# Performance work log

Measured on AMD Instinct MI355X. Metric: run time of the kernel, lower is better.

Reference implementation:

```python
import jax, jax.numpy as jnp
import numpy as np

# Multi-scale deformable attention (MSDeformableAttention from RTDETRTransformerv2)
SPATIAL = ((80, 80), (40, 40), (20, 20))  # (h, w) per level, strides 8/16/32 on 640x640
N_HEADS, N_LEVELS, N_POINTS = 8, 3, 4
D_MODEL = 256
HEAD_DIM = D_MODEL // N_HEADS


def setup_inputs() -> dict:
    key = jax.random.key(0)
    ks = jax.random.split(key, 10)
    B, Q = 16, 300
    Lv = sum(h * w for h, w in SPATIAL)  # 8400
    s = 0.02
    return {
        "query": jax.random.normal(ks[0], (B, Q, D_MODEL), jnp.float32),
        "reference_points": jax.random.uniform(ks[1], (B, Q, 4), jnp.float32),
        "value": jax.random.normal(ks[2], (B, Lv, D_MODEL), jnp.float32),
        "Wv": jax.random.normal(ks[3], (D_MODEL, D_MODEL), jnp.float32) * s,
        "bv": jnp.zeros((D_MODEL,), jnp.float32),
        "Woff": jax.random.normal(ks[4], (D_MODEL, N_HEADS * N_LEVELS * N_POINTS * 2), jnp.float32) * s,
        "boff": jax.random.normal(ks[5], (N_HEADS * N_LEVELS * N_POINTS * 2,), jnp.float32) * 0.1,
        "Wattn": jax.random.normal(ks[6], (D_MODEL, N_HEADS * N_LEVELS * N_POINTS), jnp.float32) * s,
        "battn": jnp.zeros((N_HEADS * N_LEVELS * N_POINTS,), jnp.float32),
        "Wout": jax.random.normal(ks[7], (D_MODEL, D_MODEL), jnp.float32) * s,
        "bout": jnp.zeros((D_MODEL,), jnp.float32),
    }


def _grid_sample_level(v_lvl, gx, gy, h, w):
    """Bilinear grid_sample, align_corners=False, zeros padding.

    v_lvl : (B, nH, h*w, hd) flattened per-level value map
    gx,gy : (B, nH, P) sample coords in [-1, 1]
    returns (B, nH, P, hd)
    """
    px = ((gx + 1.0) * w - 1.0) * 0.5  # pixel x
    py = ((gy + 1.0) * h - 1.0) * 0.5  # pixel y
    x0 = jnp.floor(px)
    y0 = jnp.floor(py)
    fx = px - x0
    fy = py - y0
    x0i = x0.astype(jnp.int32)
    y0i = y0.astype(jnp.int32)

    def corner(xi, yi, wgt):
        valid = (xi >= 0) & (xi < w) & (yi >= 0) & (yi < h)
        idx = jnp.clip(yi, 0, h - 1) * w + jnp.clip(xi, 0, w - 1)
        g = jnp.take_along_axis(v_lvl, idx[..., None], axis=2)  # (B,nH,P,hd)
        return g * (wgt * valid.astype(wgt.dtype))[..., None]

    return (corner(x0i, y0i, (1 - fx) * (1 - fy))
            + corner(x0i + 1, y0i, fx * (1 - fy))
            + corner(x0i, y0i + 1, (1 - fx) * fy)
            + corner(x0i + 1, y0i + 1, fx * fy))


def reference(query, reference_points, value, Wv, bv, Woff, boff, Wattn, battn, Wout, bout):
    B, Q, _ = query.shape
    # value projection -> per-head values
    v = (value @ Wv + bv).reshape(B, -1, N_HEADS, HEAD_DIM)
    # sampling offsets and attention weights from queries
    off = (query @ Woff + boff).reshape(B, Q, N_HEADS, N_LEVELS, N_POINTS, 2)
    aw = jax.nn.softmax(
        (query @ Wattn + battn).reshape(B, Q, N_HEADS, N_LEVELS * N_POINTS), axis=-1
    ).reshape(B, Q, N_HEADS, N_LEVELS, N_POINTS)
    # reference points (cx, cy) broadcast over heads/levels/points
    ref = reference_points[:, :, None, None, None, :2]
    pts = jnp.clip(ref + off, 0.0, 1.0)      # (B,Q,nH,nL,nP,2) in [0,1]
    g = pts * 2.0 - 1.0                      # grid_sample coords in [-1,1]

    out = jnp.zeros((B, Q, N_HEADS, HEAD_DIM), query.dtype)
    start = 0
    for lvl, (h, w) in enumerate(SPATIAL):
        v_lvl = v[:, start:start + h * w].transpose(0, 2, 1, 3)  # (B,nH,hw,hd)
        gl = g[:, :, :, lvl]                                     # (B,Q,nH,nP,2)
        gx = gl[..., 0].transpose(0, 2, 1, 3).reshape(B, N_HEADS, Q * N_POINTS)
        gy = gl[..., 1].transpose(0, 2, 1, 3).reshape(B, N_HEADS, Q * N_POINTS)
        sampled = _grid_sample_level(v_lvl, gx, gy, h, w)        # (B,nH,Q*nP,hd)
        sampled = sampled.reshape(B, N_HEADS, Q, N_POINTS, HEAD_DIM)
        wl = aw[:, :, :, lvl].transpose(0, 2, 1, 3)              # (B,nH,Q,nP)
        out = out + jnp.einsum('bhqpd,bhqp->bqhd', sampled, wl)
        start += h * w

    return out.reshape(B, Q, D_MODEL) @ Wout + bout
```

## Files before the change

kernel.cpp:

```cpp
#include <hip/hip_runtime.h>
#include <hip/hip_bf16.h>
#include <cstddef>

#define NB 16
#define NQ 300
#define DM 256
#define LV_ 8400

typedef __attribute__((ext_vector_type(8))) short short8;
typedef __attribute__((ext_vector_type(4))) float f32x4;

static __device__ __forceinline__ unsigned short bf16_rne(float f) {
  unsigned int u = __builtin_bit_cast(unsigned int, f);
  u += 0x7FFFu + ((u >> 16) & 1u);
  return (unsigned short)(u >> 16);
}

static __device__ __forceinline__ unsigned int pack_bf2(float a, float b) {
  __hip_bfloat162 p = __float22bfloat162_rn(make_float2(a, b));
  unsigned int u;
  __builtin_memcpy(&u, &p, 4);
  return u;
}

__global__ __launch_bounds__(256) void prep_kernel(
    const float* __restrict__ Wv, const float* __restrict__ Wout,
    unsigned short* __restrict__ Wth, unsigned short* __restrict__ WoutT) {
  const float* src = blockIdx.z ? Wout : Wv;
  unsigned short* dst = blockIdx.z ? WoutT : Wth;
  __shared__ float tle[32][33];
  const int k0 = blockIdx.x * 32, n0 = blockIdx.y * 32;
  const int xx = threadIdx.x & 31, y4 = (threadIdx.x >> 5) * 4;
  #pragma unroll
  for (int i = 0; i < 4; ++i)
    tle[y4 + i][xx] = src[(size_t)(k0 + y4 + i) * DM + n0 + xx];
  __syncthreads();
  #pragma unroll
  for (int i = 0; i < 4; ++i)
    dst[(size_t)(n0 + y4 + i) * DM + k0 + xx] = bf16_rne(tle[xx][y4 + i]);
}

__global__ __launch_bounds__(256) void vproj_mfma(
    const float* __restrict__ A, const unsigned short* __restrict__ Wth,
    const float* __restrict__ bias, unsigned short* __restrict__ V) {
  __shared__ short Ah[4][128][8];
  __shared__ short Bh[4][128][8];
  const int tid = threadIdx.x;
  const int lane = tid & 63;
  const int wave = tid >> 6;
  const int l16 = lane & 15, q4 = lane >> 4;
  const int wr = (wave >> 1) * 64, wc = (wave & 1) * 64;
  const size_t row0 = (size_t)blockIdx.x * 128;
  const int col0 = blockIdx.y * 128;

  const int arow = tid >> 1;
  const int half = tid & 1;
  const int c0 = half * 2;

  f32x4 acc[4][4];
  #pragma unroll
  for (int i = 0; i < 4; ++i)
    #pragma unroll
    for (int j = 0; j < 4; ++j) acc[i][j] = (f32x4)0.f;

  const float* ap0 = A + (row0 + arow) * DM + half * 16;
  const unsigned short* wp0 = Wth + (size_t)(col0 + arow) * DM + half * 16;

  float4 f0 = *(const float4*)(ap0 + 0);
  float4 f1 = *(const float4*)(ap0 + 4);
  float4 f2 = *(const float4*)(ap0 + 8);
  float4 f3 = *(const float4*)(ap0 + 12);
  uint4 w0 = *(const uint4*)(wp0);
  uint4 w1 = *(const uint4*)(wp0 + 8);

  for (int kk = 0; kk < DM; kk += 32) {
    uint4 p0, p1;
    p0.x = pack_bf2(f0.x, f0.y); p0.y = pack_bf2(f0.z, f0.w);
    p0.z = pack_bf2(f1.x, f1.y); p0.w = pack_bf2(f1.z, f1.w);
    p1.x = pack_bf2(f2.x, f2.y); p1.y = pack_bf2(f2.z, f2.w);
    p1.z = pack_bf2(f3.x, f3.y); p1.w = pack_bf2(f3.z, f3.w);
    uint4 cw0 = w0, cw1 = w1;
    __syncthreads();
    *(uint4*)&Ah[c0][arow][0]     = p0;
    *(uint4*)&Ah[c0 + 1][arow][0] = p1;
    *(uint4*)&Bh[c0][arow][0]     = cw0;
    *(uint4*)&Bh[c0 + 1][arow][0] = cw1;
    __syncthreads();

    if (kk + 32 < DM) {
      f0 = *(const float4*)(ap0 + kk + 32);
      f1 = *(const float4*)(ap0 + kk + 36);
      f2 = *(const float4*)(ap0 + kk + 40);
      f3 = *(const float4*)(ap0 + kk + 44);
      w0 = *(const uint4*)(wp0 + kk + 32);
      w1 = *(const uint4*)(wp0 + kk + 40);
    }

    short8 af[4], bfr[4];
    #pragma unroll
    for (int i = 0; i < 4; ++i)
      af[i] = *(const short8*)&Ah[q4][wr + i * 16 + l16][0];
    #pragma unroll
    for (int j = 0; j < 4; ++j)
      bfr[j] = *(const short8*)&Bh[q4][wc + j * 16 + l16][0];
    #pragma unroll
    for (int i = 0; i < 4; ++i)
      #pragma unroll
      for (int j = 0; j < 4; ++j)
        acc[i][j] = __builtin_amdgcn_mfma_f32_16x16x32_bf16(af[i], bfr[j], acc[i][j], 0, 0, 0);
  }

  #pragma unroll
  for (int i = 0; i < 4; ++i)
    #pragma unroll
    for (int j = 0; j < 4; ++j) {
      const int col = col0 + wc + j * 16 + l16;
      const float bcol = bias[col];
      #pragma unroll
      for (int r = 0; r < 4; ++r) {
        const size_t row = row0 + wr + i * 16 + q4 * 4 + r;
        V[row * DM + col] = bf16_rne(acc[i][j][r] + bcol);
      }
    }
}

__global__ __launch_bounds__(256) void gemm_qp(
    const float* __restrict__ q,
    const float* __restrict__ Woff, const float* __restrict__ boff,
    const float* __restrict__ Wattn, const float* __restrict__ battn,
    float* __restrict__ offb, float* __restrict__ logitb) {
  const int by = blockIdx.y;
  const float* W; const float* bias; float* C; int N, c0;
  if (by < 6) { W = Woff;  bias = boff;  C = offb;   N = 192; c0 = by * 32; }
  else        { W = Wattn; bias = battn; C = logitb; N = 96;  c0 = (by - 6) * 32; }
  const int m0 = blockIdx.x * 32;

  __shared__ float As[32][33];
  __shared__ float Bs[32][33];
  const int tid = threadIdx.x;
  const int ar = tid >> 3, ak = (tid & 7) * 4;
  const int kr = tid >> 3, bc = (tid & 7) * 4;
  const int tx = tid & 15, ty = tid >> 4;

  const float* apt = q + (size_t)(m0 + ar) * DM + ak;
  float4 av = *(const float4*)apt;
  float4 wv = *(const float4*)(W + (size_t)kr * N + c0 + bc);

  float acc[2][2] = {{0.f, 0.f}, {0.f, 0.f}};
  for (int kk = 0; kk < DM; kk += 32) {
    __syncthreads();
    As[ak + 0][ar] = av.x;
    As[ak + 1][ar] = av.y;
    As[ak + 2][ar] = av.z;
    As[ak + 3][ar] = av.w;
    *(float4*)&Bs[kr][bc] = wv;
    __syncthreads();
    if (kk + 32 < DM) {
      av = *(const float4*)(apt + kk + 32);
      wv = *(const float4*)(W + (size_t)(kk + 32 + kr) * N + c0 + bc);
    }
    #pragma unroll
    for (int k = 0; k < 32; ++k) {
      const float2 a2 = *(const float2*)&As[k][ty * 2];
      const float2 b2 = *(const float2*)&Bs[k][tx * 2];
      acc[0][0] = fmaf(a2.x, b2.x, acc[0][0]);
      acc[0][1] = fmaf(a2.x, b2.y, acc[0][1]);
      acc[1][0] = fmaf(a2.y, b2.x, acc[1][0]);
      acc[1][1] = fmaf(a2.y, b2.y, acc[1][1]);
    }
  }
  const float b0 = bias[c0 + tx * 2], b1 = bias[c0 + tx * 2 + 1];
  #pragma unroll
  for (int i = 0; i < 2; ++i) {
    float2 o; o.x = acc[i][0] + b0; o.y = acc[i][1] + b1;
    *(float2*)&C[(size_t)(m0 + ty * 2 + i) * N + c0 + tx * 2] = o;
  }
}

__global__ __launch_bounds__(256) void sample_kernel(
    const float* __restrict__ refp, const unsigned short* __restrict__ v,
    const float* __restrict__ off, const float* __restrict__ logits,
    unsigned short* __restrict__ mid) {
  const int x = blockIdx.x;
  const int c8 = x & 7, kb = x >> 3;
  const int b = c8 + (kb >= 150 ? 8 : 0);
  const int qp = (kb >= 150 ? kb - 150 : kb);
  const int bq0 = b * NQ + qp * 2;
  const int t = threadIdx.x;
  __shared__ float off_sh[2][192];
  __shared__ float aw_sh[2][96];
  __shared__ int   idx_sh[2][96][4];
  __shared__ float wt_sh[2][96][4];
  __shared__ float ref_sh[2][2];

  {
    const float* osrc = off + (size_t)bq0 * 192;
    float* odst = &off_sh[0][0];
    odst[t] = osrc[t];
    if (t < 128) odst[256 + t] = osrc[256 + t];
    const float* lsrc = logits + (size_t)bq0 * 96;
    if (t < 192) (&aw_sh[0][0])[t] = lsrc[t];
    if (t < 4) ref_sh[t >> 1][t & 1] = refp[(bq0 + (t >> 1)) * 4 + (t & 1)];
  }
  __syncthreads();

  if (t < 16) {
    const int q = t >> 3, h = t & 7;
    float* aw = &aw_sh[q][h * 12];
    float m = -1e30f;
    #pragma unroll
    for (int i = 0; i < 12; ++i) m = fmaxf(m, aw[i]);
    float e[12], s = 0.f;
    #pragma unroll
    for (int i = 0; i < 12; ++i) { e[i] = __expf(aw[i] - m); s += e[i]; }
    const float inv = 1.f / s;
    #pragma unroll
    for (int i = 0; i < 12; ++i) aw[i] = e[i] * inv;
  }
  __syncthreads();

  if (t < 192) {
    const int q = t / 96, r = t - q * 96;
    const int h = r / 12, lp = r - h * 12;
    const int l = lp >> 2, p = lp & 3;
    const int LH[3] = {80, 40, 20};
    const int LS[3] = {0, 6400, 8000};
    const int hh = LH[l], ww = LH[l], st = LS[l];
    const int oi = ((h * 3 + l) * 4 + p) * 2;
    const float aw = aw_sh[q][h * 12 + lp];
    const float sx = fminf(fmaxf(ref_sh[q][0] + off_sh[q][oi], 0.f), 1.f);
    const float sy = fminf(fmaxf(ref_sh[q][1] + off_sh[q][oi + 1], 0.f), 1.f);
    const float px = sx * (float)ww - 0.5f;
    const float py = sy * (float)hh - 0.5f;
    const float x0f = floorf(px), y0f = floorf(py);
    const float fx = px - x0f, fy = py - y0f;
    const int x0 = (int)x0f, y0 = (int)y0f;
    const int x1 = x0 + 1, y1 = y0 + 1;
    const bool vx0 = (x0 >= 0) & (x0 < ww), vx1 = (x1 >= 0) & (x1 < ww);
    const bool vy0 = (y0 >= 0) & (y0 < hh), vy1 = (y1 >= 0) & (y1 < hh);
    const int x0c = min(max(x0, 0), ww - 1), x1c = min(max(x1, 0), ww - 1);
    const int y0c = min(max(y0, 0), hh - 1), y1c = min(max(y1, 0), hh - 1);
    idx_sh[q][r][0] = st + y0c * ww + x0c;
    idx_sh[q][r][1] = st + y0c * ww + x1c;
    idx_sh[q][r][2] = st + y1c * ww + x0c;
    idx_sh[q][r][3] = st + y1c * ww + x1c;
    wt_sh[q][r][0] = aw * (1.f - fx) * (1.f - fy) * ((vx0 & vy0) ? 1.f : 0.f);
    wt_sh[q][r][1] = aw * fx * (1.f - fy) * ((vx1 & vy0) ? 1.f : 0.f);
    wt_sh[q][r][2] = aw * (1.f - fx) * fy * ((vx0 & vy1) ? 1.f : 0.f);
    wt_sh[q][r][3] = aw * fx * fy * ((vx1 & vy1) ? 1.f : 0.f);
  }
  __syncthreads();

  const int q = t >> 7, h = (t >> 4) & 7, dp = t & 15;
  const unsigned short* vb = v + (size_t)b * LV_ * DM + h * 32 + dp * 2;
  float ax = 0.f, ay = 0.f;
  #pragma unroll
  for (int r = 0; r < 12; ++r) {
    const int rr = h * 12 + r;
    #pragma unroll
    for (int cc = 0; cc < 4; ++cc) {
      const int id = idx_sh[q][rr][cc];
      const float w = wt_sh[q][rr][cc];
      const unsigned int u = *(const unsigned int*)(vb + (size_t)id * DM);
      ax = fmaf(w, __builtin_bit_cast(float, u << 16), ax);
      ay = fmaf(w, __builtin_bit_cast(float, u & 0xFFFF0000u), ay);
    }
  }
  unsigned short* mp = mid + (size_t)(bq0 + q) * DM + h * 32 + dp * 2;
  *(unsigned int*)mp = pack_bf2(ax, ay);
}

__global__ __launch_bounds__(256) void outp_mfma(
    const unsigned short* __restrict__ midb, const unsigned short* __restrict__ WoutT,
    const float* __restrict__ bias, float* __restrict__ out) {
  __shared__ short Ah[4][64][8];
  __shared__ short Bh[4][64][8];
  const int tid = threadIdx.x;
  const int lane = tid & 63;
  const int wave = tid >> 6;
  const int l16 = lane & 15, q4 = lane >> 4;
  const int wc = wave * 16;
  const int m0 = blockIdx.x * 64, col0 = blockIdx.y * 64;

  const int r = tid >> 2, ch = tid & 3;
  const unsigned short* apt = midb + (size_t)(m0 + r) * DM + ch * 8;
  const unsigned short* wpt = WoutT + (size_t)(col0 + r) * DM + ch * 8;
  uint4 am = *(const uint4*)apt;
  uint4 wm = *(const uint4*)wpt;

  f32x4 acc[4];
  #pragma unroll
  for (int i = 0; i < 4; ++i) acc[i] = (f32x4)0.f;

  for (int kk = 0; kk < DM; kk += 32) {
    __syncthreads();
    *(uint4*)&Ah[ch][r][0] = am;
    *(uint4*)&Bh[ch][r][0] = wm;
    __syncthreads();
    if (kk + 32 < DM) {
      am = *(const uint4*)(apt + kk + 32);
      wm = *(const uint4*)(wpt + kk + 32);
    }
    const short8 bfrag = *(const short8*)&Bh[q4][wc + l16][0];
    #pragma unroll
    for (int i = 0; i < 4; ++i) {
      const short8 af = *(const short8*)&Ah[q4][i * 16 + l16][0];
      acc[i] = __builtin_amdgcn_mfma_f32_16x16x32_bf16(af, bfrag, acc[i], 0, 0, 0);
    }
  }

  const int col = col0 + wc + l16;
  const float bcol = bias[col];
  #pragma unroll
  for (int i = 0; i < 4; ++i)
    #pragma unroll
    for (int rr = 0; rr < 4; ++rr)
      out[(size_t)(m0 + i * 16 + q4 * 4 + rr) * DM + col] = acc[i][rr] + bcol;
}

extern "C" void kernel_launch(void* const* d_in, const int* in_sizes, int n_in,
                              void* d_out, int out_size, void* d_ws, size_t ws_size,
                              hipStream_t stream) {
  (void)in_sizes; (void)n_in; (void)out_size; (void)ws_size;
  const float* query = (const float*)d_in[0];
  const float* refp  = (const float*)d_in[1];
  const float* value = (const float*)d_in[2];
  const float* Wv    = (const float*)d_in[3];
  const float* bv    = (const float*)d_in[4];
  const float* Woff  = (const float*)d_in[5];
  const float* boff  = (const float*)d_in[6];
  const float* Wattn = (const float*)d_in[7];
  const float* battn = (const float*)d_in[8];
  const float* Wout  = (const float*)d_in[9];
  const float* bout  = (const float*)d_in[10];
  float* out = (float*)d_out;

  char* ws = (char*)d_ws;
  unsigned short* v_bf  = (unsigned short*)ws;
  unsigned short* Wth   = (unsigned short*)(ws + 68812800);
  unsigned short* WoutT = (unsigned short*)(ws + 68943872);
  float* offb   = (float*)(ws + 69074944);
  float* logitb = (float*)(ws + 72761344);
  unsigned short* midb = (unsigned short*)(ws + 74604544);

  prep_kernel<<<dim3(8, 8, 2), 256, 0, stream>>>(Wv, Wout, Wth, WoutT);
  gemm_qp<<<dim3(150, 9), 256, 0, stream>>>(query, Woff, boff, Wattn, battn, offb, logitb);
  vproj_mfma<<<dim3((NB * LV_) / 128, 2), 256, 0, stream>>>(value, Wth, bv, v_bf);
  sample_kernel<<<2400, 256, 0, stream>>>(refp, v_bf, offb, logitb, midb);
  outp_mfma<<<dim3(75, 4), 256, 0, stream>>>(midb, WoutT, bout, out);
}
```

Baseline: 296.2 us.

## Stream value GEMM tiles via global_load_lds double buffering with prepacked weights

Rewrites the value projection GEMM to copy fp32 A tiles and pre-packed bf16 weight tiles straight from global memory into LDS with async global_load_lds, double-buffered across K steps. The fp32-to-bf16 conversion moves to after the LDS read, and an XOR swizzle is used to limit bank conflicts. The prep kernel now writes Wv in the packed per-K-block layout the loader expects. Blocks are remapped to a flattened grid with XCD-aware ordering so neighbouring tiles share L2. This doubles LDS use (fp32 A staging) and adds packing work inside the inner loop.

Result: no change. 291.4 us (-1.6%).

```diff
diff --git a/kernel.cpp b/kernel.cpp
--- a/kernel.cpp
+++ b/kernel.cpp
@@ -23,39 +23,79 @@
   return u;
 }
 
+static __device__ __forceinline__ void gload16(const void* g, void* l) {
+  __builtin_amdgcn_global_load_lds(
+      (const __attribute__((address_space(1))) unsigned int*)g,
+      (__attribute__((address_space(3))) unsigned int*)l, 16, 0, 0);
+}
+
 __global__ __launch_bounds__(256) void prep_kernel(
     const float* __restrict__ Wv, const float* __restrict__ Wout,
-    unsigned short* __restrict__ Wth, unsigned short* __restrict__ WoutT) {
-  const float* src = blockIdx.z ? Wout : Wv;
-  unsigned short* dst = blockIdx.z ? WoutT : Wth;
+    unsigned short* __restrict__ WthP, unsigned short* __restrict__ WoutT) {
   __shared__ float tle[32][33];
   const int k0 = blockIdx.x * 32, n0 = blockIdx.y * 32;
   const int xx = threadIdx.x & 31, y4 = (threadIdx.x >> 5) * 4;
+  const float* src = blockIdx.z ? Wout : Wv;
   #pragma unroll
   for (int i = 0; i < 4; ++i)
     tle[y4 + i][xx] = src[(size_t)(k0 + y4 + i) * DM + n0 + xx];
   __syncthreads();
-  #pragma unroll
-  for (int i = 0; i < 4; ++i)
-    dst[(size_t)(n0 + y4 + i) * DM + k0 + xx] = bf16_rne(tle[xx][y4 + i]);
-}
-
-__global__ __launch_bounds__(256) void vproj_mfma(
-    const float* __restrict__ A, const unsigned short* __restrict__ Wth,
+  if (blockIdx.z == 0) {
+    if (threadIdx.x < 128) {
+      const int nl = threadIdx.x >> 2, q8 = threadIdx.x & 3;
+      const int n = n0 + nl, yy = n >> 7, col = n & 127;
+      uint4 o;
+      o.x = pack_bf2(tle[q8 * 8 + 0][nl], tle[q8 * 8 + 1][nl]);
+      o.y = pack_bf2(tle[q8 * 8 + 2][nl], tle[q8 * 8 + 3][nl]);
+      o.z = pack_bf2(tle[q8 * 8 + 4][nl], tle[q8 * 8 + 5][nl]);
+      o.w = pack_bf2(tle[q8 * 8 + 6][nl], tle[q8 * 8 + 7][nl]);
+      const size_t idx = ((((size_t)yy * 8 + blockIdx.x) * 4 + q8) * 128 + col) * 8;
+      *(uint4*)&WthP[idx] = o;
+    }
+  } else {
+    #pragma unroll
+    for (int i = 0; i < 4; ++i)
+      WoutT[(size_t)(n0 + y4 + i) * DM + k0 + xx] = bf16_rne(tle[xx][y4 + i]);
+  }
+}
+
+__global__ __launch_bounds__(256, 3) void vproj_mfma(
+    const float* __restrict__ A, const unsigned short* __restrict__ WthP,
     const float* __restrict__ bias, unsigned short* __restrict__ V) {
-  __shared__ short Ah[4][128][8];
-  __shared__ short Bh[4][128][8];
+  __shared__ float Af[2][4][128][8];
+  __shared__ unsigned short Bf[2][4][128][8];
   const int tid = threadIdx.x;
   const int lane = tid & 63;
   const int wave = tid >> 6;
   const int l16 = lane & 15, q4 = lane >> 4;
   const int wr = (wave >> 1) * 64, wc = (wave & 1) * 64;
-  const size_t row0 = (size_t)blockIdx.x * 128;
-  const int col0 = blockIdx.y * 128;
-
-  const int arow = tid >> 1;
-  const int half = tid & 1;
-  const int c0 = half * 2;
+
+  const int b = blockIdx.x;
+  const int xcd = b & 7, cidx = b >> 3;
+  const int w = (xcd < 4 ? xcd * 263 : 4 * 263 + (xcd - 4) * 262) + cidx;
+  const int xb = w >> 1, y = w & 1;
+  const size_t row0 = (size_t)xb * 128;
+  const int col0 = y * 128;
+
+  const unsigned short* bsrc = WthP + (size_t)y * 8 * 4096;
+
+#define STAGE(bufi, kb_) do {                                                  \
+    _Pragma("unroll")                                                          \
+    for (int c_ = 0; c_ < 4; ++c_) {                                           \
+      const int u_ = wave * 4 + c_;                                            \
+      const int row_ = c_ * 32 + (lane >> 1);                                  \
+      const int h_ = lane & 1;                                                 \
+      const int k_ = wave * 8 + ((h_ ^ ((row_ >> 2) & 1)) << 2);               \
+      gload16(A + (row0 + row_) * DM + (kb_) * 32 + k_,                        \
+              (char*)&Af[bufi][0][0][0] + u_ * 1024);                          \
+    }                                                                          \
+    _Pragma("unroll")                                                          \
+    for (int c_ = 0; c_ < 2; ++c_) {                                           \
+      const int u_ = wave * 2 + c_;                                            \
+      gload16(bsrc + (size_t)(kb_) * 4096 + u_ * 512 + lane * 8,               \
+              (char*)&Bf[bufi][0][0][0] + u_ * 1024);                          \
+    }                                                                          \
+  } while (0)
 
   f32x4 acc[4][4];
   #pragma unroll
@@ -63,52 +103,37 @@
     #pragma unroll
     for (int j = 0; j < 4; ++j) acc[i][j] = (f32x4)0.f;
 
-  const float* ap0 = A + (row0 + arow) * DM + half * 16;
-  const unsigned short* wp0 = Wth + (size_t)(col0 + arow) * DM + half * 16;
-
-  float4 f0 = *(const float4*)(ap0 + 0);
-  float4 f1 = *(const float4*)(ap0 + 4);
-  float4 f2 = *(const float4*)(ap0 + 8);
-  float4 f3 = *(const float4*)(ap0 + 12);
-  uint4 w0 = *(const uint4*)(wp0);
-  uint4 w1 = *(const uint4*)(wp0 + 8);
-
-  for (int kk = 0; kk < DM; kk += 32) {
-    uint4 p0, p1;
-    p0.x = pack_bf2(f0.x, f0.y); p0.y = pack_bf2(f0.z, f0.w);
-    p0.z = pack_bf2(f1.x, f1.y); p0.w = pack_bf2(f1.z, f1.w);
-    p1.x = pack_bf2(f2.x, f2.y); p1.y = pack_bf2(f2.z, f2.w);
-    p1.z = pack_bf2(f3.x, f3.y); p1.w = pack_bf2(f3.z, f3.w);
-    uint4 cw0 = w0, cw1 = w1;
-    __syncthreads();
-    *(uint4*)&Ah[c0][arow][0]     = p0;
-    *(uint4*)&Ah[c0 + 1][arow][0] = p1;
-    *(uint4*)&Bh[c0][arow][0]     = cw0;
-    *(uint4*)&Bh[c0 + 1][arow][0] = cw1;
-    __syncthreads();
-
-    if (kk + 32 < DM) {
-      f0 = *(const float4*)(ap0 + kk + 32);
-      f1 = *(const float4*)(ap0 + kk + 36);
-      f2 = *(const float4*)(ap0 + kk + 40);
-      f3 = *(const float4*)(ap0 + kk + 44);
-      w0 = *(const uint4*)(wp0 + kk + 32);
-      w1 = *(const uint4*)(wp0 + kk + 40);
-    }
-
-    short8 af[4], bfr[4];
-    #pragma unroll
-    for (int i = 0; i < 4; ++i)
-      af[i] = *(const short8*)&Ah[q4][wr + i * 16 + l16][0];
+  const int swf = ((l16 >> 2) & 1) << 2;
+
+  int buf = 0;
+  STAGE(0, 0);
+  __syncthreads();
+
+  for (int kb = 0; kb < 8; ++kb) {
+    if (kb < 7) STAGE(buf ^ 1, kb + 1);
+
+    short8 bfr[4];
     #pragma unroll
     for (int j = 0; j < 4; ++j)
-      bfr[j] = *(const short8*)&Bh[q4][wc + j * 16 + l16][0];
-    #pragma unroll
-    for (int i = 0; i < 4; ++i)
+      bfr[j] = *(const short8*)&Bf[buf][q4][wc + j * 16 + l16][0];
+
+    #pragma unroll
+    for (int i = 0; i < 4; ++i) {
+      const float* rp = &Af[buf][q4][wr + i * 16 + l16][0];
+      const float4 lo = *(const float4*)(rp + swf);
+      const float4 hi = *(const float4*)(rp + (4 ^ swf));
+      uint4 p;
+      p.x = pack_bf2(lo.x, lo.y); p.y = pack_bf2(lo.z, lo.w);
+      p.z = pack_bf2(hi.x, hi.y); p.w = pack_bf2(hi.z, hi.w);
+      const short8 af = __builtin_bit_cast(short8, p);
       #pragma unroll
       for (int j = 0; j < 4; ++j)
-        acc[i][j] = __builtin_amdgcn_mfma_f32_16x16x32_bf16(af[i], bfr[j], acc[i][j], 0, 0, 0);
-  }
+        acc[i][j] = __builtin_amdgcn_mfma_f32_16x16x32_bf16(af, bfr[j], acc[i][j], 0, 0, 0);
+    }
+    __syncthreads();
+    buf ^= 1;
+  }
+#undef STAGE
 
   #pragma unroll
   for (int i = 0; i < 4; ++i)
@@ -337,15 +362,15 @@
 
   char* ws = (char*)d_ws;
   unsigned short* v_bf  = (unsigned short*)ws;
-  unsigned short* Wth   = (unsigned short*)(ws + 68812800);
+  unsigned short* WthP  = (unsigned short*)(ws + 68812800);
   unsigned short* WoutT = (unsigned short*)(ws + 68943872);
   float* offb   = (float*)(ws + 69074944);
   float* logitb = (float*)(ws + 72761344);
   unsigned short* midb = (unsigned short*)(ws + 74604544);
 
-  prep_kernel<<<dim3(8, 8, 2), 256, 0, stream>>>(Wv, Wout, Wth, WoutT);
+  prep_kernel<<<dim3(8, 8, 2), 256, 0, stream>>>(Wv, Wout, WthP, WoutT);
   gemm_qp<<<dim3(150, 9), 256, 0, stream>>>(query, Woff, boff, Wattn, battn, offb, logitb);
-  vproj_mfma<<<dim3((NB * LV_) / 128, 2), 256, 0, stream>>>(value, Wth, bv, v_bf);
+  vproj_mfma<<<2100, 256, 0, stream>>>(value, WthP, bv, v_bf);
   sample_kernel<<<2400, 256, 0, stream>>>(refp, v_bf, offb, logitb, midb);
   outp_mfma<<<dim3(75, 4), 256, 0, stream>>>(midb, WoutT, bout, out);
 }
```
